# Kernel tuning notes

Hardware: AMD Instinct MI355X
Metric: run time of the kernel (lower is better)

## Reference

```python
import math
import jax, jax.numpy as jnp
import numpy as np

N, D = 16384, 1024


def setup_inputs() -> dict:
    key = jax.random.key(0)
    k1, k2 = jax.random.split(key)
    return {
        "image_embeddings_aligned": jax.random.normal(k1, (N, D), dtype=jnp.float32),
        "text_embeddings_aligned": jax.random.normal(k2, (N, D), dtype=jnp.float32),
        "logit_scale": jnp.asarray(math.log(20.0), dtype=jnp.float32),  # stored as log(init)
        "logit_bias": jnp.asarray(-10.0, dtype=jnp.float32),
    }


def _l2_normalize(x, eps=1e-12):
    # matches F.normalize(p=2, dim=-1)
    n = jnp.linalg.norm(x, axis=-1, keepdims=True)
    return x / jnp.maximum(n, eps)


def reference(image_embeddings_aligned, text_embeddings_aligned, logit_scale, logit_bias):
    img = _l2_normalize(image_embeddings_aligned)
    txt = _l2_normalize(text_embeddings_aligned)
    # [N, N] pairwise logits
    logits = jnp.exp(logit_scale) * jnp.einsum("nd,md->nm", img, txt) + logit_bias
    n = logits.shape[0]
    labels = 2.0 * jnp.eye(n, dtype=logits.dtype) - 1.0  # +1 on diagonal, -1 off
    loss_matrix = jax.nn.log_sigmoid(labels * logits)
    siglip_loss = -jnp.mean(loss_matrix)  # total_loss (structure_lambda == 0)
    return siglip_loss
```

## Files before the change

kernel.cpp:

```cpp
#include <hip/hip_runtime.h>

#define NROWS 16384
#define DIM   1024
#define QSCALE 32.0f
#define E8M0S  0x7A7A7A7Au

typedef int    v4i    __attribute__((ext_vector_type(4)));
typedef int    v8i    __attribute__((ext_vector_type(8)));
typedef float  f32x16 __attribute__((ext_vector_type(16)));

__device__ __forceinline__ void glds16(const void* g, void* l) {
    __builtin_amdgcn_global_load_lds(
        (const __attribute__((address_space(1))) void*)g,
        (__attribute__((address_space(3))) void*)l,
        16, 0, 0);
}

__device__ __forceinline__ float fexp2(float x) {
#if __has_builtin(__builtin_amdgcn_exp2f)
    return __builtin_amdgcn_exp2f(x);
#else
    return exp2f(x);
#endif
}
__device__ __forceinline__ float flog2(float x) {
#if __has_builtin(__builtin_amdgcn_logf)
    return __builtin_amdgcn_logf(x);
#else
    return log2f(x);
#endif
}

__device__ __forceinline__ unsigned fp4_nib(float y) {
    unsigned s = (__float_as_uint(y) >> 31) << 3;
    float a = fminf(fabsf(y), 6.0f);
    unsigned c = (unsigned)(a >= 0.25f) + (unsigned)(a >= 0.75f) +
                 (unsigned)(a >= 1.25f) + (unsigned)(a >= 1.75f) +
                 (unsigned)(a >= 2.5f)  + (unsigned)(a >= 3.5f)  +
                 (unsigned)(a >= 5.0f);
    return c | s;
}

__global__ __launch_bounds__(256) void norm_fused(
    const float* __restrict__ img,
    const float* __restrict__ txt,
    unsigned char* __restrict__ imgQ,
    unsigned char* __restrict__ txtQ,
    const float* __restrict__ lscale,
    const float* __restrict__ lbias,
    float* __restrict__ diagPart) {
    const int t    = threadIdx.x;
    const int lane = t & 63;
    const int wave = t >> 6;
    const int gw   = blockIdx.x * 4 + wave;
    const float sc   = __expf(lscale[0]);
    const float bias = lbias[0];

    for (int row = gw; row < NROWS; row += 8192) {
        const float4* pi = (const float4*)(img + (size_t)row * DIM);
        const float4* pt = (const float4*)(txt + (size_t)row * DIM);
        float4 vi[4], vt[4];
        float ssi = 0.0f, sst = 0.0f, dot = 0.0f;
        #pragma unroll
        for (int j = 0; j < 4; ++j) {
            vi[j] = pi[lane + 64 * j];
            vt[j] = pt[lane + 64 * j];
            ssi += vi[j].x*vi[j].x + vi[j].y*vi[j].y + vi[j].z*vi[j].z + vi[j].w*vi[j].w;
            sst += vt[j].x*vt[j].x + vt[j].y*vt[j].y + vt[j].z*vt[j].z + vt[j].w*vt[j].w;
            dot += vi[j].x*vt[j].x + vi[j].y*vt[j].y + vi[j].z*vt[j].z + vi[j].w*vt[j].w;
        }
        #pragma unroll
        for (int off = 1; off < 64; off <<= 1) {
            ssi += __shfl_xor(ssi, off, 64);
            sst += __shfl_xor(sst, off, 64);
            dot += __shfl_xor(dot, off, 64);
        }
        const float ii = 1.0f / fmaxf(sqrtf(ssi), 1e-12f);
        const float it = 1.0f / fmaxf(sqrtf(sst), 1e-12f);
        if (lane == 0) diagPart[row] = -fmaf(sc, dot * ii * it, bias);

        const float qi = ii * QSCALE, qt = it * QSCALE;
        ushort* oi = (ushort*)(imgQ + (size_t)row * 512);
        ushort* ot = (ushort*)(txtQ + (size_t)row * 512);
        #pragma unroll
        for (int j = 0; j < 4; ++j) {
            unsigned p = fp4_nib(vi[j].x * qi)        | (fp4_nib(vi[j].y * qi) << 4) |
                         (fp4_nib(vi[j].z * qi) << 8) | (fp4_nib(vi[j].w * qi) << 12);
            unsigned q = fp4_nib(vt[j].x * qt)        | (fp4_nib(vt[j].y * qt) << 4) |
                         (fp4_nib(vt[j].z * qt) << 8) | (fp4_nib(vt[j].w * qt) << 12);
            oi[lane + 64 * j] = (ushort)p;
            ot[lane + 64 * j] = (ushort)q;
        }
    }
}

__global__ __launch_bounds__(256, 4) void siglip_gemm(
    const unsigned char* __restrict__ A,
    const unsigned char* __restrict__ B,
    const float* __restrict__ lscale,
    const float* __restrict__ lbias,
    float* __restrict__ gemmPart)
{
    __shared__ unsigned char sA[128 * 128];
    __shared__ unsigned char sB[128 * 128];
    __shared__ float wred[4];

    const int t    = threadIdx.x;
    const int lane = t & 63;
    const int wave = t >> 6;
    const int wr   = wave >> 1;
    const int wc   = wave & 1;
    const int r31  = lane & 31;
    const int h    = lane >> 5;
    const int xr   = (r31 & 7) ^ ((r31 >> 4) & 1);

    const int b    = blockIdx.x;
    const int xcd  = b & 7;
    const int lb   = b >> 3;
    const int bcol = xcd * 16 + (lb & 15);
    const int brow = lb >> 4;

    const size_t aBase = (size_t)brow * 128;
    const size_t bBase = (size_t)bcol * 128;

    const int srow = lane >> 3;
    const int c0   = (lane & 7) ^ srow;
    const int d01  = (c0 & 1) ? -16 : 16;

    const unsigned char* aP = A + (size_t)(aBase + wave * 32 + srow) * 512 + c0 * 16;
    const unsigned char* bP = B + (size_t)(bBase + wave * 32 + srow) * 512 + c0 * 16;
    char* la  = ((char*)sA) + wave * 4096;
    char* lbp = ((char*)sB) + wave * 4096;

    int rbA[2], rbB[2];
    #pragma unroll
    for (int i = 0; i < 2; ++i) rbA[i] = (wr * 64 + i * 32 + r31) * 128;
    #pragma unroll
    for (int i = 0; i < 2; ++i) rbB[i] = (wc * 64 + i * 32 + r31) * 128;

    f32x16 acc[2][2] = {};

    #pragma unroll
    for (int j = 0; j < 4; ++j) {
        const int tog = ((j >> 1) & 1) ? d01 : 0;
        glds16(aP + j * 4096 + tog, la + j * 1024);
        glds16(bP + j * 4096 + tog, lbp + j * 1024);
    }
    __syncthreads();

    #pragma unroll
    for (int k = 0; k < 4; ++k) {
        #pragma unroll
        for (int ks = 0; ks < 4; ++ks) {
            const int s = ((ks * 2 + h) ^ xr) * 16;
            v4i a0 = *(const v4i*)(sA + rbA[0] + s);
            v4i a1 = *(const v4i*)(sA + rbA[1] + s);
            v4i b0 = *(const v4i*)(sB + rbB[0] + s);
            v4i b1 = *(const v4i*)(sB + rbB[1] + s);
            v8i A0 = __builtin_shufflevector(a0, a0, 0, 1, 2, 3, -1, -1, -1, -1);
            v8i A1 = __builtin_shufflevector(a1, a1, 0, 1, 2, 3, -1, -1, -1, -1);
            v8i B0 = __builtin_shufflevector(b0, b0, 0, 1, 2, 3, -1, -1, -1, -1);
            v8i B1 = __builtin_shufflevector(b1, b1, 0, 1, 2, 3, -1, -1, -1, -1);
            __builtin_amdgcn_s_setprio(1);
            acc[0][0] = __builtin_amdgcn_mfma_scale_f32_32x32x64_f8f6f4(
                A0, B0, acc[0][0], 4, 4, 0, (int)E8M0S, 0, (int)E8M0S);
            acc[0][1] = __builtin_amdgcn_mfma_scale_f32_32x32x64_f8f6f4(
                A0, B1, acc[0][1], 4, 4, 0, (int)E8M0S, 0, (int)E8M0S);
            acc[1][0] = __builtin_amdgcn_mfma_scale_f32_32x32x64_f8f6f4(
                A1, B0, acc[1][0], 4, 4, 0, (int)E8M0S, 0, (int)E8M0S);
            acc[1][1] = __builtin_amdgcn_mfma_scale_f32_32x32x64_f8f6f4(
                A1, B1, acc[1][1], 4, 4, 0, (int)E8M0S, 0, (int)E8M0S);
            __builtin_amdgcn_s_setprio(0);
        }

        if (k < 3) {
            __syncthreads();
            const unsigned char* aN = aP + (k + 1) * 128;
            const unsigned char* bN = bP + (k + 1) * 128;
            #pragma unroll
            for (int j = 0; j < 4; ++j) {
                const int tog = ((j >> 1) & 1) ? d01 : 0;
                glds16(aN + j * 4096 + tog, la + j * 1024);
                glds16(bN + j * 4096 + tog, lbp + j * 1024);
            }
            __syncthreads();
        }
    }

    const float l2e   = 1.44269504088896341f;
    const float scale = __expf(lscale[0]);
    const float aCo   = scale * l2e;
    const float bCo   = lbias[0] * l2e;
    float local = 0.0f;
    #pragma unroll
    for (int mi = 0; mi < 2; ++mi)
        #pragma unroll
        for (int ni = 0; ni < 2; ++ni)
            #pragma unroll
            for (int r = 0; r < 16; r += 4) {
                float e0 = fexp2(fmaf(aCo, acc[mi][ni][r + 0], bCo));
                float e1 = fexp2(fmaf(aCo, acc[mi][ni][r + 1], bCo));
                float e2 = fexp2(fmaf(aCo, acc[mi][ni][r + 2], bCo));
                float e3 = fexp2(fmaf(aCo, acc[mi][ni][r + 3], bCo));
                float p  = ((1.0f + e0) * (1.0f + e1)) *
                           ((1.0f + e2) * (1.0f + e3));
                local += flog2(p);
            }

    #pragma unroll
    for (int off = 32; off > 0; off >>= 1) local += __shfl_down(local, off, 64);
    if (lane == 0) wred[wave] = local;
    __syncthreads();
    if (t == 0)
        gemmPart[blockIdx.x] =
            (wred[0] + wred[1] + wred[2] + wred[3]) * 0.69314718055994531f;
}

__global__ __launch_bounds__(1024) void finalize_kernel(
    const float* __restrict__ parts, float* __restrict__ out) {
    __shared__ float wr[16];
    const int t    = threadIdx.x;
    const int lane = t & 63;
    const int wave = t >> 6;
    const float4* p4 = (const float4*)parts;
    float s = 0.0f;
    for (int i = t; i < 8192; i += 1024) {
        float4 v = p4[i];
        s += v.x + v.y + v.z + v.w;
    }
    #pragma unroll
    for (int off = 32; off > 0; off >>= 1) s += __shfl_down(s, off, 64);
    if (lane == 0) wr[wave] = s;
    __syncthreads();
    if (t == 0) {
        float tot = 0.0f;
        #pragma unroll
        for (int i = 0; i < 16; ++i) tot += wr[i];
        out[0] = tot / 268435456.0f;
    }
}

extern "C" void kernel_launch(void* const* d_in, const int* in_sizes, int n_in,
                              void* d_out, int out_size, void* d_ws, size_t ws_size,
                              hipStream_t stream) {
    const float* img    = (const float*)d_in[0];
    const float* txt    = (const float*)d_in[1];
    const float* lscale = (const float*)d_in[2];
    const float* lbias  = (const float*)d_in[3];
    float* out = (float*)d_out;

    char* ws = (char*)d_ws;
    unsigned char* imgQ = (unsigned char*)ws;
    unsigned char* txtQ = (unsigned char*)(ws + (size_t)NROWS * 512);
    float* parts   = (float*)(ws + (size_t)2 * NROWS * 512);
    float* diagPart = parts;
    float* gemmPart = parts + NROWS;

    norm_fused<<<2048, 256, 0, stream>>>(img, txt, imgQ, txtQ, lscale, lbias, diagPart);
    siglip_gemm<<<dim3((NROWS / 128) * (NROWS / 128)), 256, 0, stream>>>(
        imgQ, txtQ, lscale, lbias, gemmPart);
    finalize_kernel<<<1, 1024, 0, stream>>>(parts, out);
}
```

Baseline: 310.2 us.

## Pre-swizzle FP4 operands into MFMA fragment layout and load B directly to registers

The normalize/quantize kernel now handles two rows per wave and writes FP4 data in a blocked layout that matches the per-lane MFMA fragment order, using one 16-byte store per lane. The GEMM then reads B fragments straight from global memory into registers with one-step prefetch, and double-buffers only the A tile in LDS, which removes one of the two barriers per k-step and the XOR swizzle arithmetic. The aim is to cut LDS traffic, barrier stalls and address math. In exchange, B is re-read from global or L2 by each wave pair instead of being shared through LDS, and global-load latency sits closer to the MFMA chain.

```diff
diff --git a/kernel.cpp b/kernel.cpp
--- a/kernel.cpp
+++ b/kernel.cpp
@@ -51,47 +51,49 @@
     float* __restrict__ diagPart) {
     const int t    = threadIdx.x;
     const int lane = t & 63;
-    const int wave = t >> 6;
-    const int gw   = blockIdx.x * 4 + wave;
+    const int r31  = lane & 31;
+    const int half = lane >> 5;
+    const int gw   = blockIdx.x * 4 + (t >> 6);
+    const int row  = gw * 2 + half;
     const float sc   = __expf(lscale[0]);
     const float bias = lbias[0];
 
-    for (int row = gw; row < NROWS; row += 8192) {
-        const float4* pi = (const float4*)(img + (size_t)row * DIM);
-        const float4* pt = (const float4*)(txt + (size_t)row * DIM);
-        float4 vi[4], vt[4];
-        float ssi = 0.0f, sst = 0.0f, dot = 0.0f;
-        #pragma unroll
-        for (int j = 0; j < 4; ++j) {
-            vi[j] = pi[lane + 64 * j];
-            vt[j] = pt[lane + 64 * j];
-            ssi += vi[j].x*vi[j].x + vi[j].y*vi[j].y + vi[j].z*vi[j].z + vi[j].w*vi[j].w;
-            sst += vt[j].x*vt[j].x + vt[j].y*vt[j].y + vt[j].z*vt[j].z + vt[j].w*vt[j].w;
-            dot += vi[j].x*vt[j].x + vi[j].y*vt[j].y + vi[j].z*vt[j].z + vi[j].w*vt[j].w;
-        }
-        #pragma unroll
-        for (int off = 1; off < 64; off <<= 1) {
-            ssi += __shfl_xor(ssi, off, 64);
-            sst += __shfl_xor(sst, off, 64);
-            dot += __shfl_xor(dot, off, 64);
-        }
-        const float ii = 1.0f / fmaxf(sqrtf(ssi), 1e-12f);
-        const float it = 1.0f / fmaxf(sqrtf(sst), 1e-12f);
-        if (lane == 0) diagPart[row] = -fmaf(sc, dot * ii * it, bias);
-
-        const float qi = ii * QSCALE, qt = it * QSCALE;
-        ushort* oi = (ushort*)(imgQ + (size_t)row * 512);
-        ushort* ot = (ushort*)(txtQ + (size_t)row * 512);
-        #pragma unroll
-        for (int j = 0; j < 4; ++j) {
-            unsigned p = fp4_nib(vi[j].x * qi)        | (fp4_nib(vi[j].y * qi) << 4) |
-                         (fp4_nib(vi[j].z * qi) << 8) | (fp4_nib(vi[j].w * qi) << 12);
-            unsigned q = fp4_nib(vt[j].x * qt)        | (fp4_nib(vt[j].y * qt) << 4) |
-                         (fp4_nib(vt[j].z * qt) << 8) | (fp4_nib(vt[j].w * qt) << 12);
-            oi[lane + 64 * j] = (ushort)p;
-            ot[lane + 64 * j] = (ushort)q;
-        }
-    }
+    const float4* pi = (const float4*)(img + (size_t)row * DIM) + r31 * 8;
+    const float4* pt = (const float4*)(txt + (size_t)row * DIM) + r31 * 8;
+    float4 vi[8], vt[8];
+    float ssi = 0.0f, sst = 0.0f, dot = 0.0f;
+    #pragma unroll
+    for (int j = 0; j < 8; ++j) {
+        vi[j] = pi[j];
+        vt[j] = pt[j];
+        ssi += vi[j].x*vi[j].x + vi[j].y*vi[j].y + vi[j].z*vi[j].z + vi[j].w*vi[j].w;
+        sst += vt[j].x*vt[j].x + vt[j].y*vt[j].y + vt[j].z*vt[j].z + vt[j].w*vt[j].w;
+        dot += vi[j].x*vt[j].x + vi[j].y*vt[j].y + vi[j].z*vt[j].z + vi[j].w*vt[j].w;
+    }
+    #pragma unroll
+    for (int off = 1; off < 32; off <<= 1) {
+        ssi += __shfl_xor(ssi, off, 64);
+        sst += __shfl_xor(sst, off, 64);
+        dot += __shfl_xor(dot, off, 64);
+    }
+    const float ii = 1.0f / fmaxf(sqrtf(ssi), 1e-12f);
+    const float it = 1.0f / fmaxf(sqrtf(sst), 1e-12f);
+    if (r31 == 0) diagPart[row] = -fmaf(sc, dot * ii * it, bias);
+
+    const float qi = ii * QSCALE, qt = it * QSCALE;
+    unsigned wp[4] = {0, 0, 0, 0}, wq[4] = {0, 0, 0, 0};
+    #pragma unroll
+    for (int j = 0; j < 8; ++j) {
+        unsigned p = fp4_nib(vi[j].x * qi)       | (fp4_nib(vi[j].y * qi) << 4) |
+                     (fp4_nib(vi[j].z * qi) << 8) | (fp4_nib(vi[j].w * qi) << 12);
+        unsigned q = fp4_nib(vt[j].x * qt)       | (fp4_nib(vt[j].y * qt) << 4) |
+                     (fp4_nib(vt[j].z * qt) << 8) | (fp4_nib(vt[j].w * qt) << 12);
+        wp[j >> 1] |= p << ((j & 1) * 16);
+        wq[j >> 1] |= q << ((j & 1) * 16);
+    }
+    const size_t qoff = ((size_t)(row >> 5) * 32 + r31) * 512 + (row & 31) * 16;
+    *(v4i*)(imgQ + qoff) = *(v4i*)wp;
+    *(v4i*)(txtQ + qoff) = *(v4i*)wq;
 }
 
 __global__ __launch_bounds__(256, 4) void siglip_gemm(
@@ -101,8 +103,7 @@
     const float* __restrict__ lbias,
     float* __restrict__ gemmPart)
 {
-    __shared__ unsigned char sA[128 * 128];
-    __shared__ unsigned char sB[128 * 128];
+    __shared__ unsigned char sA[2][16 * 1024];
     __shared__ float wred[4];
 
     const int t    = threadIdx.x;
@@ -110,9 +111,6 @@
     const int wave = t >> 6;
     const int wr   = wave >> 1;
     const int wc   = wave & 1;
-    const int r31  = lane & 31;
-    const int h    = lane >> 5;
-    const int xr   = (r31 & 7) ^ ((r31 >> 4) & 1);
 
     const int b    = blockIdx.x;
     const int xcd  = b & 7;
@@ -120,47 +118,47 @@
     const int bcol = xcd * 16 + (lb & 15);
     const int brow = lb >> 4;
 
-    const size_t aBase = (size_t)brow * 128;
-    const size_t bBase = (size_t)bcol * 128;
-
-    const int srow = lane >> 3;
-    const int c0   = (lane & 7) ^ srow;
-    const int d01  = (c0 & 1) ? -16 : 16;
-
-    const unsigned char* aP = A + (size_t)(aBase + wave * 32 + srow) * 512 + c0 * 16;
-    const unsigned char* bP = B + (size_t)(bBase + wave * 32 + srow) * 512 + c0 * 16;
-    char* la  = ((char*)sA) + wave * 4096;
-    char* lbp = ((char*)sB) + wave * 4096;
-
-    int rbA[2], rbB[2];
-    #pragma unroll
-    for (int i = 0; i < 2; ++i) rbA[i] = (wr * 64 + i * 32 + r31) * 128;
-    #pragma unroll
-    for (int i = 0; i < 2; ++i) rbB[i] = (wc * 64 + i * 32 + r31) * 128;
+    const unsigned char* Aw = A + ((size_t)(brow * 4 + wave) * 32) * 512
+                                + (size_t)lane * 16;
+    const unsigned char* Bw = B + ((size_t)(bcol * 4 + wc * 2) * 32) * 512
+                                + (size_t)lane * 16;
 
     f32x16 acc[2][2] = {};
 
     #pragma unroll
-    for (int j = 0; j < 4; ++j) {
-        const int tog = ((j >> 1) & 1) ? d01 : 0;
-        glds16(aP + j * 4096 + tog, la + j * 1024);
-        glds16(bP + j * 4096 + tog, lbp + j * 1024);
-    }
+    for (int s = 0; s < 4; ++s)
+        glds16(Aw + (size_t)(s * 2) * 512, sA[0] + (wave * 8 + s * 2) * 512);
     __syncthreads();
 
     #pragma unroll
     for (int k = 0; k < 4; ++k) {
+        const int cur = k & 1;
+
+        if (k < 3) {
+            #pragma unroll
+            for (int s = 0; s < 4; ++s)
+                glds16(Aw + (size_t)((k + 1) * 8 + s * 2) * 512,
+                       sA[cur ^ 1] + (wave * 8 + s * 2) * 512);
+        }
+
+        v4i bc0 = *(const v4i*)(Bw + (size_t)(k * 8) * 512);
+        v4i bc1 = *(const v4i*)(Bw + 16384 + (size_t)(k * 8) * 512);
+
         #pragma unroll
         for (int ks = 0; ks < 4; ++ks) {
-            const int s = ((ks * 2 + h) ^ xr) * 16;
-            v4i a0 = *(const v4i*)(sA + rbA[0] + s);
-            v4i a1 = *(const v4i*)(sA + rbA[1] + s);
-            v4i b0 = *(const v4i*)(sB + rbB[0] + s);
-            v4i b1 = *(const v4i*)(sB + rbB[1] + s);
+            v4i bn0, bn1;
+            if (ks < 3) {
+                bn0 = *(const v4i*)(Bw + (size_t)(k * 8 + (ks + 1) * 2) * 512);
+                bn1 = *(const v4i*)(Bw + 16384 + (size_t)(k * 8 + (ks + 1) * 2) * 512);
+            }
+            v4i a0 = *(const v4i*)(sA[cur] + ((2 * wr + 0) * 8 + ks * 2) * 512 + lane * 16);
+            v4i a1 = *(const v4i*)(sA[cur] + ((2 * wr + 1) * 8 + ks * 2) * 512 + lane * 16);
+
             v8i A0 = __builtin_shufflevector(a0, a0, 0, 1, 2, 3, -1, -1, -1, -1);
             v8i A1 = __builtin_shufflevector(a1, a1, 0, 1, 2, 3, -1, -1, -1, -1);
-            v8i B0 = __builtin_shufflevector(b0, b0, 0, 1, 2, 3, -1, -1, -1, -1);
-            v8i B1 = __builtin_shufflevector(b1, b1, 0, 1, 2, 3, -1, -1, -1, -1);
+            v8i B0 = __builtin_shufflevector(bc0, bc0, 0, 1, 2, 3, -1, -1, -1, -1);
+            v8i B1 = __builtin_shufflevector(bc1, bc1, 0, 1, 2, 3, -1, -1, -1, -1);
+
             __builtin_amdgcn_s_setprio(1);
             acc[0][0] = __builtin_amdgcn_mfma_scale_f32_32x32x64_f8f6f4(
                 A0, B0, acc[0][0], 4, 4, 0, (int)E8M0S, 0, (int)E8M0S);
@@ -171,20 +169,11 @@
             acc[1][1] = __builtin_amdgcn_mfma_scale_f32_32x32x64_f8f6f4(
                 A1, B1, acc[1][1], 4, 4, 0, (int)E8M0S, 0, (int)E8M0S);
             __builtin_amdgcn_s_setprio(0);
+
+            if (ks < 3) { bc0 = bn0; bc1 = bn1; }
         }
 
-        if (k < 3) {
-            __syncthreads();
-            const unsigned char* aN = aP + (k + 1) * 128;
-            const unsigned char* bN = bP + (k + 1) * 128;
-            #pragma unroll
-            for (int j = 0; j < 4; ++j) {
-                const int tog = ((j >> 1) & 1) ? d01 : 0;
-                glds16(aN + j * 4096 + tog, la + j * 1024);
-                glds16(bN + j * 4096 + tog, lbp + j * 1024);
-            }
-            __syncthreads();
-        }
+        __syncthreads();
     }
 
     const float l2e   = 1.44269504088896341f;
```

Measured after the change: 313.1 us. About the same (+0.9%).
